# Optimization experiments

Measured on AMD Instinct MI355X. Metric: run time of the kernel, lower is better.

The kernel has to match this reference:

```python
import jax, jax.numpy as jnp
import numpy as np

D_MODEL = 1024
BATCH = 4
SEQ = 4096

def setup_inputs() -> dict:
    key = jax.random.key(0)
    k1, k2, k3, k4 = jax.random.split(key, 4)
    scale = 1.0 / np.sqrt(D_MODEL)
    return {
        "inp_emb": jax.random.normal(k1, (BATCH, SEQ, D_MODEL), dtype=jnp.float32),
        "Wq": jax.random.normal(k2, (D_MODEL, D_MODEL), dtype=jnp.float32) * scale,
        "Wk": jax.random.normal(k3, (D_MODEL, D_MODEL), dtype=jnp.float32) * scale,
        "Wv": jax.random.normal(k4, (D_MODEL, D_MODEL), dtype=jnp.float32) * scale,
    }

def reference(inp_emb, Wq, Wk, Wv):
    d_model = Wq.shape[0]
    # torch Linear (no bias): y = x @ W.T
    Q = jnp.einsum('bsd,ed->bse', inp_emb, Wq)
    K = jnp.einsum('bsd,ed->bse', inp_emb, Wk)
    V = jnp.einsum('bsd,ed->bse', inp_emb, Wv)
    scores = jnp.einsum('bqd,bkd->bqk', Q, K) / jnp.sqrt(jnp.float32(d_model))
    probs = jax.nn.softmax(scores, axis=2)
    return jnp.einsum('bqk,bkd->bqd', probs, V)
```

## Files before the change

kernel.cpp:

```cpp
#include <hip/hip_runtime.h>


typedef __bf16 bf16_t;
typedef __bf16 bf16x8 __attribute__((ext_vector_type(8)));
typedef float f32x4 __attribute__((ext_vector_type(4)));

typedef __attribute__((address_space(3))) void lds_void_t;
typedef __attribute__((address_space(1))) void gbl_void_t;

#define SEQ 4096
#define DM  1024

__global__ __launch_bounds__(256) void cast_f32_to_bf16(
    const float* __restrict__ in, bf16_t* __restrict__ out, int n8)
{
    int idx = blockIdx.x * 256 + threadIdx.x;
    if (idx >= n8) return;
    long i = (long)idx * 8;
    f32x4 a = *(const f32x4*)(in + i);
    f32x4 b = *(const f32x4*)(in + i + 4);
    bf16x8 o;
    o[0] = (bf16_t)a[0]; o[1] = (bf16_t)a[1]; o[2] = (bf16_t)a[2]; o[3] = (bf16_t)a[3];
    o[4] = (bf16_t)b[0]; o[5] = (bf16_t)b[1]; o[6] = (bf16_t)b[2]; o[7] = (bf16_t)b[3];
    *(bf16x8*)(out + i) = o;
}

__global__ __launch_bounds__(256) void cast3_w(
    const float* __restrict__ w0, const float* __restrict__ w1,
    const float* __restrict__ w2, bf16_t* __restrict__ out)
{
    const float* in = (blockIdx.z == 0) ? w0 : (blockIdx.z == 1) ? w1 : w2;
    long i = ((long)blockIdx.x * 256 + threadIdx.x) * 8;
    f32x4 a = *(const f32x4*)(in + i);
    f32x4 b = *(const f32x4*)(in + i + 4);
    bf16x8 o;
    o[0] = (bf16_t)a[0]; o[1] = (bf16_t)a[1]; o[2] = (bf16_t)a[2]; o[3] = (bf16_t)a[3];
    o[4] = (bf16_t)b[0]; o[5] = (bf16_t)b[1]; o[6] = (bf16_t)b[2]; o[7] = (bf16_t)b[3];
    *(bf16x8*)(out + (long)blockIdx.z * 1048576 + i) = o;
}

__global__ __launch_bounds__(256) void zero_f32(float* __restrict__ p, int n)
{
    int idx = blockIdx.x * 256 + threadIdx.x;
    if (idx < n) p[idx] = 0.f;
}

template <typename TOUT, int MODE>
__global__ __launch_bounds__(256, 4) void gemm_bt(
    const bf16_t* __restrict__ A, int lda, long sAz,
    const bf16_t* __restrict__ B, int ldb, long sBz,
    TOUT* __restrict__ C, int ldc, long sCz,
    int K, float scale, float* __restrict__ l, long sLz)
{
    __shared__ bf16_t As[128 * 32];
    __shared__ bf16_t Bs[128 * 32];

    A += (long)blockIdx.z * sAz;
    B += (long)blockIdx.z * sBz;
    C += (long)blockIdx.z * sCz;

    const int tid  = threadIdx.x;
    const int wave = tid >> 6;
    const int lane = tid & 63;
    const int m0 = blockIdx.x * 128;
    const int n0 = blockIdx.y * 128;
    const int wm = (wave >> 1) * 64;
    const int wn = (wave & 1) * 64;
    const int mrow = lane & 15;
    const int koff = (lane >> 4) * 8;

    f32x4 acc[4][4];
#pragma unroll
    for (int i = 0; i < 4; ++i)
#pragma unroll
        for (int j = 0; j < 4; ++j)
            acc[i][j] = (f32x4){0.f, 0.f, 0.f, 0.f};

    const int c0 = wave * 2;

    for (int k0 = 0; k0 < K; k0 += 32) {
#pragma unroll
        for (int t = 0; t < 2; ++t) {
            const int chunk = c0 + t;
            const int flat  = chunk * 64 + lane;
            const int row   = flat >> 2;
            const int kp    = (flat & 3) * 8;
            const bf16_t* ga = A + (long)(m0 + row) * lda + (k0 + kp);
            const bf16_t* gb = B + (long)(n0 + row) * ldb + (k0 + kp);
            __builtin_amdgcn_global_load_lds((const gbl_void_t*)ga,
                                             (lds_void_t*)(As + chunk * 512), 16, 0, 0);
            __builtin_amdgcn_global_load_lds((const gbl_void_t*)gb,
                                             (lds_void_t*)(Bs + chunk * 512), 16, 0, 0);
        }
        __syncthreads();

        bf16x8 af[4], bfr[4];
#pragma unroll
        for (int i = 0; i < 4; ++i)
            af[i] = *(const bf16x8*)(As + (wm + i * 16 + mrow) * 32 + koff);
#pragma unroll
        for (int j = 0; j < 4; ++j)
            bfr[j] = *(const bf16x8*)(Bs + (wn + j * 16 + mrow) * 32 + koff);
#pragma unroll
        for (int i = 0; i < 4; ++i)
#pragma unroll
            for (int j = 0; j < 4; ++j)
                acc[i][j] = __builtin_amdgcn_mfma_f32_16x16x32_bf16(af[i], bfr[j], acc[i][j], 0, 0, 0);
        __syncthreads();
    }

    const int col = lane & 15;
    const int r0  = (lane >> 4) * 4;

    if (MODE == 1) {
#pragma unroll
        for (int i = 0; i < 4; ++i)
#pragma unroll
            for (int r = 0; r < 4; ++r) {
                float s = 0.f;
#pragma unroll
                for (int j = 0; j < 4; ++j) {
                    float e = __expf(acc[i][j][r] * scale);
                    acc[i][j][r] = e;
                    s += e;
                }
                s += __shfl_xor(s, 1);
                s += __shfl_xor(s, 2);
                s += __shfl_xor(s, 4);
                s += __shfl_xor(s, 8);
                if (col == 0)
                    atomicAdd(&l[(long)blockIdx.z * sLz + m0 + wm + i * 16 + r0 + r], s);
            }
#pragma unroll
        for (int i = 0; i < 4; ++i)
#pragma unroll
            for (int j = 0; j < 4; ++j)
#pragma unroll
                for (int r = 0; r < 4; ++r)
                    C[(long)(m0 + wm + i * 16 + r0 + r) * ldc + (n0 + wn + j * 16 + col)] =
                        (TOUT)acc[i][j][r];
    } else if (MODE == 2) {
        float inv[4][4];
#pragma unroll
        for (int i = 0; i < 4; ++i)
#pragma unroll
            for (int r = 0; r < 4; ++r)
                inv[i][r] = scale / l[(long)blockIdx.z * sLz + m0 + wm + i * 16 + r0 + r];
#pragma unroll
        for (int i = 0; i < 4; ++i)
#pragma unroll
            for (int j = 0; j < 4; ++j)
#pragma unroll
                for (int r = 0; r < 4; ++r)
                    C[(long)(m0 + wm + i * 16 + r0 + r) * ldc + (n0 + wn + j * 16 + col)] =
                        (TOUT)(acc[i][j][r] * inv[i][r]);
    } else {
#pragma unroll
        for (int i = 0; i < 4; ++i)
#pragma unroll
            for (int j = 0; j < 4; ++j)
#pragma unroll
                for (int r = 0; r < 4; ++r)
                    C[(long)(m0 + wm + i * 16 + r0 + r) * ldc + (n0 + wn + j * 16 + col)] =
                        (TOUT)(acc[i][j][r] * scale);
    }
}

template <typename TOUT, int MODE, int LDA, int LDB, int LDC>
__global__ __launch_bounds__(512, 4) void gemm_bt256(
    const bf16_t* __restrict__ A, long sAz,
    const bf16_t* __restrict__ B, long sBz,
    TOUT* __restrict__ C, long sCz,
    int K, float scale, float* __restrict__ l, long sLz)
{
    __shared__ __align__(1024) char smem[73728];

    A += (long)blockIdx.z * sAz;
    B += (long)blockIdx.z * sBz;
    C += (long)blockIdx.z * sCz;

    const int tid  = threadIdx.x;
    const int wave = tid >> 6;
    const int lane = tid & 63;
    const int m0 = blockIdx.x * 256;
    const int n0 = blockIdx.y * 128;
    const int wm = (wave >> 2) * 128;
    const int wn = (wave & 3) * 32;

    const int srow = wave * 16 + (lane >> 2);
    const int ksrc = (((lane & 3) ^ ((lane >> 3) & 3)) << 3);
    const bf16_t* pa0 = A + (long)(m0 + srow) * LDA + ksrc;
    const bf16_t* pa1 = pa0 + (long)128 * LDA;
    const bf16_t* pb0 = B + (long)(n0 + srow) * LDB + ksrc;
    const int ldsw = wave * 1024;

    const int kterm = (((lane >> 4) ^ ((lane >> 1) & 3)) << 4);
    const int aoff = (wm + (lane & 15)) * 64 + kterm;
    const int boff = (wn + (lane & 15)) * 64 + kterm;

    f32x4 acc[8][2];
#pragma unroll
    for (int i = 0; i < 8; ++i)
#pragma unroll
        for (int j = 0; j < 2; ++j)
            acc[i][j] = (f32x4){0.f, 0.f, 0.f, 0.f};

    const int NT = K >> 5;

#define STAGE_A2(buf)                                                          \
    do {                                                                       \
        __builtin_amdgcn_global_load_lds((const gbl_void_t*)pa0,               \
            (lds_void_t*)(smem + (buf)*16384 + ldsw), 16, 0, 0);               \
        __builtin_amdgcn_global_load_lds((const gbl_void_t*)pa1,               \
            (lds_void_t*)(smem + (buf)*16384 + 8192 + ldsw), 16, 0, 0);        \
    } while (0)
#define STAGE_B1(buf)                                                          \
    __builtin_amdgcn_global_load_lds((const gbl_void_t*)pb0,                   \
        (lds_void_t*)(smem + 49152 + (buf)*8192 + ldsw), 16, 0, 0)

    STAGE_A2(0); STAGE_B1(0); pa0 += 32; pa1 += 32; pb0 += 32;
    if (NT > 1) {
        STAGE_A2(1); STAGE_B1(1); pa0 += 32; pa1 += 32; pb0 += 32;
        asm volatile("s_waitcnt vmcnt(3)" ::: "memory");
    } else {
        asm volatile("s_waitcnt vmcnt(0)" ::: "memory");
    }
    __builtin_amdgcn_sched_barrier(0);
    __builtin_amdgcn_s_barrier();

    int cur = 0, sb = 2;
    for (int t = 0; t < NT; ++t) {
        const char* Ab = smem + cur * 16384;
        const char* Bb = smem + 49152 + cur * 8192;
        const bool more = (t + 2 < NT);

        bf16x8 bfr[2], af[4];
#pragma unroll
        for (int j = 0; j < 2; ++j) bfr[j] = *(const bf16x8*)(Bb + boff + j * 1024);
#pragma unroll
        for (int i = 0; i < 4; ++i) af[i] = *(const bf16x8*)(Ab + aoff + i * 1024);
        if (more) STAGE_A2(sb);
        asm volatile("s_waitcnt lgkmcnt(0)" ::: "memory");
        __builtin_amdgcn_sched_barrier(0);
        __builtin_amdgcn_s_setprio(1);
#pragma unroll
        for (int i = 0; i < 4; ++i)
#pragma unroll
            for (int j = 0; j < 2; ++j)
                acc[i][j] = __builtin_amdgcn_mfma_f32_16x16x32_bf16(af[i], bfr[j], acc[i][j], 0, 0, 0);
        __builtin_amdgcn_s_setprio(0);

#pragma unroll
        for (int i = 0; i < 4; ++i) af[i] = *(const bf16x8*)(Ab + aoff + 4096 + i * 1024);
        if (more) STAGE_B1(sb);
        asm volatile("s_waitcnt lgkmcnt(0)" ::: "memory");
        __builtin_amdgcn_sched_barrier(0);
        __builtin_amdgcn_s_setprio(1);
#pragma unroll
        for (int i = 0; i < 4; ++i)
#pragma unroll
            for (int j = 0; j < 2; ++j)
                acc[4 + i][j] = __builtin_amdgcn_mfma_f32_16x16x32_bf16(af[i], bfr[j], acc[4 + i][j], 0, 0, 0);
        __builtin_amdgcn_s_setprio(0);

        if (more) {
            asm volatile("s_waitcnt vmcnt(3)" ::: "memory");
            pa0 += 32; pa1 += 32; pb0 += 32;
        } else if (t + 1 < NT) {
            asm volatile("s_waitcnt vmcnt(0)" ::: "memory");
        }
        __builtin_amdgcn_sched_barrier(0);
        __builtin_amdgcn_s_barrier();
        cur = (cur == 2) ? 0 : cur + 1;
        sb  = (sb == 2) ? 0 : sb + 1;
    }
#undef STAGE_A2
#undef STAGE_B1

    const int col = lane & 15;
    const int r0  = (lane >> 4) * 4;

    if (MODE == 1) {
#pragma unroll
        for (int i = 0; i < 8; ++i)
#pragma unroll
            for (int r = 0; r < 4; ++r) {
                float s = 0.f;
#pragma unroll
                for (int j = 0; j < 2; ++j) {
                    float e = __expf(acc[i][j][r] * scale);
                    acc[i][j][r] = e;
                    s += e;
                }
                s += __shfl_xor(s, 1);
                s += __shfl_xor(s, 2);
                s += __shfl_xor(s, 4);
                s += __shfl_xor(s, 8);
                if (col == 0)
                    atomicAdd(&l[(long)blockIdx.z * sLz + m0 + wm + i * 16 + r0 + r], s);
            }
#pragma unroll
        for (int i = 0; i < 8; ++i)
#pragma unroll
            for (int j = 0; j < 2; ++j)
#pragma unroll
                for (int r = 0; r < 4; ++r)
                    C[(long)(m0 + wm + i * 16 + r0 + r) * LDC + (n0 + wn + j * 16 + col)] =
                        (TOUT)acc[i][j][r];
    } else if (MODE == 2) {
        float inv[8][4];
#pragma unroll
        for (int i = 0; i < 8; ++i)
#pragma unroll
            for (int r = 0; r < 4; ++r)
                inv[i][r] = scale / l[(long)blockIdx.z * sLz + m0 + wm + i * 16 + r0 + r];
#pragma unroll
        for (int i = 0; i < 8; ++i)
#pragma unroll
            for (int j = 0; j < 2; ++j)
#pragma unroll
                for (int r = 0; r < 4; ++r)
                    C[(long)(m0 + wm + i * 16 + r0 + r) * LDC + (n0 + wn + j * 16 + col)] =
                        (TOUT)(acc[i][j][r] * inv[i][r]);
    } else {
#pragma unroll
        for (int i = 0; i < 8; ++i)
#pragma unroll
            for (int j = 0; j < 2; ++j)
#pragma unroll
                for (int r = 0; r < 4; ++r)
                    C[(long)(m0 + wm + i * 16 + r0 + r) * LDC + (n0 + wn + j * 16 + col)] =
                        (TOUT)(acc[i][j][r] * scale);
    }
}

__device__ __forceinline__ float waveMax(float v)
{
#pragma unroll
    for (int o = 32; o > 0; o >>= 1) v = fmaxf(v, __shfl_xor(v, o));
    return v;
}
__device__ __forceinline__ float waveSum(float v)
{
#pragma unroll
    for (int o = 32; o > 0; o >>= 1) v += __shfl_xor(v, o);
    return v;
}

__global__ __launch_bounds__(256) void softmax_rows(bf16_t* __restrict__ S)
{
    const long row = blockIdx.x;
    bf16_t* p = S + row * SEQ;
    const int tid = threadIdx.x;

    float v[16];
    bf16x8 a0 = *(const bf16x8*)(p + tid * 16);
    bf16x8 a1 = *(const bf16x8*)(p + tid * 16 + 8);
#pragma unroll
    for (int i = 0; i < 8; ++i) { v[i] = (float)a0[i]; v[8 + i] = (float)a1[i]; }

    float m = -1e30f;
#pragma unroll
    for (int i = 0; i < 16; ++i) m = fmaxf(m, v[i]);

    __shared__ float redm[4];
    __shared__ float reds[4];
    m = waveMax(m);
    if ((tid & 63) == 0) redm[tid >> 6] = m;
    __syncthreads();
    m = fmaxf(fmaxf(redm[0], redm[1]), fmaxf(redm[2], redm[3]));

    float s = 0.f;
#pragma unroll
    for (int i = 0; i < 16; ++i) { v[i] = __expf(v[i] - m); s += v[i]; }
    s = waveSum(s);
    if ((tid & 63) == 0) reds[tid >> 6] = s;
    __syncthreads();
    s = reds[0] + reds[1] + reds[2] + reds[3];
    const float inv = 1.0f / s;

    bf16x8 o0, o1;
#pragma unroll
    for (int i = 0; i < 8; ++i) {
        o0[i] = (bf16_t)(v[i] * inv);
        o1[i] = (bf16_t)(v[8 + i] * inv);
    }
    *(bf16x8*)(p + tid * 16)     = o0;
    *(bf16x8*)(p + tid * 16 + 8) = o1;
}

__global__ __launch_bounds__(256) void transpose_bf16(
    const bf16_t* __restrict__ in, int ldin, long sInZ,
    bf16_t* __restrict__ out, int ldout, long sOutZ)
{
    in  += (long)blockIdx.z * sInZ;
    out += (long)blockIdx.z * sOutZ;
    __shared__ bf16_t t[32][33];
    const int tx = threadIdx.x;
    const int ty = threadIdx.y;
    const int x  = blockIdx.x * 32 + tx;
    const int y0 = blockIdx.y * 32;
#pragma unroll
    for (int i = 0; i < 4; ++i)
        t[ty + i * 8][tx] = in[(long)(y0 + ty + i * 8) * ldin + x];
    __syncthreads();
    const int xo = blockIdx.x * 32;
#pragma unroll
    for (int i = 0; i < 4; ++i)
        out[(long)(xo + ty + i * 8) * ldout + y0 + tx] = t[tx][ty + i * 8];
}

extern "C" void kernel_launch(void* const* d_in, const int* in_sizes, int n_in,
                              void* d_out, int out_size, void* d_ws, size_t ws_size,
                              hipStream_t stream)
{
    const float* X  = (const float*)d_in[0];
    const float* Wq = (const float*)d_in[1];
    const float* Wk = (const float*)d_in[2];
    const float* Wv = (const float*)d_in[3];
    float* out = (float*)d_out;
    char* ws = (char*)d_ws;

    if (ws_size >= (256ull << 20)) {
        bf16_t* Xbf  = (bf16_t*)ws;
        bf16_t* Vbf  = (bf16_t*)(ws + (32l << 20));
        bf16_t* Tbuf = (bf16_t*)(ws + (32l << 20));
        bf16_t* VT   = (bf16_t*)(ws + (64l << 20));
        bf16_t* Sbuf = (bf16_t*)(ws + (96l << 20));
        bf16_t* Wall = (bf16_t*)(ws + (224l << 20));
        bf16_t* WqT  = (bf16_t*)(ws + (230l << 20));
        bf16_t* WkT  = (bf16_t*)(ws + (232l << 20));
        bf16_t* Mt   = (bf16_t*)(ws + (234l << 20));
        float*  lbuf = (float*)(ws + (236l << 20));

        cast_f32_to_bf16<<<(16777216 / 8) / 256, 256, 0, stream>>>(X, Xbf, 16777216 / 8);
        cast3_w<<<dim3(512, 1, 3), 256, 0, stream>>>(Wq, Wk, Wv, Wall);

        transpose_bf16<<<dim3(32, 32, 2), dim3(32, 8), 0, stream>>>(
            Wall, DM, 1048576, WqT, DM, 1048576);

        gemm_bt<bf16_t, 0><<<dim3(8, 8, 1), 256, 0, stream>>>(
            WkT, DM, 0l, WqT, DM, 0l, Mt, DM, 0l, DM, 1.0f, nullptr, 0l);

        gemm_bt256<bf16_t, 0, DM, DM, DM><<<dim3(64, 8, 1), 512, 0, stream>>>(
            Xbf, 0l, Wall + 2097152, 0l, Vbf, 0l, DM, 1.0f, nullptr, 0l);

        transpose_bf16<<<dim3(DM / 32, SEQ / 32, 4), dim3(32, 8), 0, stream>>>(
            Vbf, DM, (long)SEQ * DM, VT, SEQ, (long)DM * SEQ);

        gemm_bt256<bf16_t, 0, DM, DM, DM><<<dim3(64, 8, 1), 512, 0, stream>>>(
            Xbf, 0l, Mt, 0l, Tbuf, 0l, DM, 1.0f, nullptr, 0l);

        zero_f32<<<64, 256, 0, stream>>>(lbuf, 4 * SEQ);

        gemm_bt256<bf16_t, 1, DM, DM, SEQ><<<dim3(16, 32, 4), 512, 0, stream>>>(
            Tbuf, (long)SEQ * DM,
            Xbf, (long)SEQ * DM,
            Sbuf, (long)SEQ * SEQ, DM, 0.03125f, lbuf, SEQ);

        gemm_bt256<float, 2, SEQ, SEQ, DM><<<dim3(16, 8, 4), 512, 0, stream>>>(
            Sbuf, (long)SEQ * SEQ,
            VT, (long)DM * SEQ,
            out, (long)SEQ * DM, SEQ, 1.0f, lbuf, SEQ);
    } else {
        bf16_t* Sbuf = (bf16_t*)ws;
        bf16_t* Xbf  = (bf16_t*)ws;
        bf16_t* Wall = (bf16_t*)(ws + (33l << 20));
        bf16_t* QKV  = (bf16_t*)(ws + (40l << 20));
        bf16_t* VT   = (bf16_t*)(ws + (137l << 20));

        cast_f32_to_bf16<<<(16777216 / 8) / 256, 256, 0, stream>>>(X, Xbf, 16777216 / 8);
        cast3_w<<<dim3(512, 1, 3), 256, 0, stream>>>(Wq, Wk, Wv, Wall);

        gemm_bt<bf16_t, 0><<<dim3(128, 24, 1), 256, 0, stream>>>(
            Xbf, DM, 0l, Wall, DM, 0l, QKV, 3072, 0l, DM, 1.0f, nullptr, 0l);

        for (int b = 0; b < 4; ++b) {
            const bf16_t* Qb = QKV + (long)b * SEQ * 3072;
            gemm_bt<bf16_t, 0><<<dim3(32, 32, 1), 256, 0, stream>>>(
                Qb, 3072, 0l, Qb + 1024, 3072, 0l, Sbuf, SEQ, 0l, DM, 0.03125f, nullptr, 0l);
            softmax_rows<<<SEQ, 256, 0, stream>>>(Sbuf);
            transpose_bf16<<<dim3(DM / 32, SEQ / 32, 1), dim3(32, 8), 0, stream>>>(
                Qb + 2048, 3072, 0l, VT, SEQ, 0l);
            gemm_bt<float, 0><<<dim3(32, 8, 1), 256, 0, stream>>>(
                Sbuf, SEQ, 0l, VT, SEQ, 0l, out + (long)b * SEQ * DM, DM, 0l, SEQ, 1.0f, nullptr, 0l);
        }
    }
}
```

Measured before the change: 545.7 us.

## Add 256x256 projection GEMM computing V transposed directly, swizzle block order

Adds a new 256x256-tile double-buffered projection GEMM kernel with direct global-to-LDS loads. It computes V^T directly as Wv·X^T per batch, which removes the separate V projection write plus transpose pass. It also uses this kernel for the X·M projection and adds a grouped workgroup-order swizzle to the existing 256x128 GEMM to improve L2 reuse. The costs are larger LDS use (128KB, lower occupancy) and strided output writes for VT.

```diff
diff --git a/kernel.cpp b/kernel.cpp
--- a/kernel.cpp
+++ b/kernel.cpp
@@ -166,6 +166,160 @@
     }
 }
 
+__global__ __launch_bounds__(512, 2) void gemm_proj(
+    const bf16_t* __restrict__ A, int lda, long sAz,
+    const bf16_t* __restrict__ B, int ldb, long sBz,
+    bf16_t* __restrict__ C, int ldc, long sCz,
+    int K, float scale)
+{
+    __shared__ __align__(1024) char smem[131072];
+
+    A += (long)blockIdx.z * sAz;
+    B += (long)blockIdx.z * sBz;
+    C += (long)blockIdx.z * sCz;
+
+    const int wg  = blockIdx.y * gridDim.x + blockIdx.x;
+    const int qq  = (gridDim.x * gridDim.y) >> 3;
+    const int sw  = (wg & 7) * qq + (wg >> 3);
+    const int m0 = (sw % gridDim.x) * 256;
+    const int n0 = (sw / gridDim.x) * 256;
+
+    const int tid  = threadIdx.x;
+    const int wave = tid >> 6;
+    const int lane = tid & 63;
+    const int wm = (wave >> 2) * 128;
+    const int wn = (wave & 3) * 64;
+
+    const int ksw = ((lane & 7) ^ (lane >> 3)) * 8;
+    const bf16_t* gAr = A + (long)(m0 + wave * 8 + (lane >> 3)) * lda + ksw;
+    const bf16_t* gBr = B + (long)(n0 + wave * 8 + (lane >> 3)) * ldb + ksw;
+    const int ldsw = wave * 1024;
+
+    const int kterm = ((lane >> 4) * 16) ^ ((lane & 7) << 4);
+    const int aoff = (wm + (lane & 15)) * 128 + kterm;
+    const int boff = (wn + (lane & 15)) * 128 + kterm;
+
+    f32x4 acc[8][4];
+#pragma unroll
+    for (int i = 0; i < 8; ++i)
+#pragma unroll
+        for (int j = 0; j < 4; ++j)
+            acc[i][j] = (f32x4){0.f, 0.f, 0.f, 0.f};
+
+    const int NT = K >> 6;
+
+#define STAGE_A(buf, k0e, s)                                                   \
+    __builtin_amdgcn_global_load_lds(                                          \
+        (const gbl_void_t*)(gAr + (long)(s)*64 * lda + (k0e)),                 \
+        (lds_void_t*)(smem + (buf)*32768 + (s)*8192 + ldsw), 16, 0, 0)
+#define STAGE_B(buf, k0e, s)                                                   \
+    __builtin_amdgcn_global_load_lds(                                          \
+        (const gbl_void_t*)(gBr + (long)(s)*64 * ldb + (k0e)),                 \
+        (lds_void_t*)(smem + 65536 + (buf)*32768 + (s)*8192 + ldsw), 16, 0, 0)
+
+    STAGE_B(0, 0, 0); STAGE_B(0, 0, 1); STAGE_B(0, 0, 2); STAGE_B(0, 0, 3);
+    STAGE_A(0, 0, 0); STAGE_A(0, 0, 2); STAGE_A(0, 0, 1); STAGE_A(0, 0, 3);
+    asm volatile("s_waitcnt vmcnt(2)" ::: "memory");
+    __builtin_amdgcn_sched_barrier(0);
+    __builtin_amdgcn_s_barrier();
+
+    for (int t = 0; t < NT; ++t) {
+        const int cb = t & 1;
+        const int nb = cb ^ 1;
+        const char* Ac = smem + cb * 32768;
+        const char* Bc = smem + 65536 + cb * 32768;
+        const bool more = (t + 1 < NT);
+        const int kn = (t + 1) << 6;
+
+        bf16x8 b0[4], b1[4], af[4];
+
+#pragma unroll
+        for (int j = 0; j < 4; ++j) b0[j] = *(const bf16x8*)(Bc + boff + j * 2048);
+#pragma unroll
+        for (int i = 0; i < 4; ++i) af[i] = *(const bf16x8*)(Ac + aoff + i * 2048);
+        if (more) { STAGE_B(nb, kn, 0); STAGE_B(nb, kn, 1); }
+        __builtin_amdgcn_s_barrier();
+        asm volatile("s_waitcnt lgkmcnt(0)" ::: "memory");
+        __builtin_amdgcn_sched_barrier(0);
+        __builtin_amdgcn_s_setprio(1);
+#pragma unroll
+        for (int i = 0; i < 4; ++i)
+#pragma unroll
+            for (int j = 0; j < 4; ++j)
+                acc[i][j] = __builtin_amdgcn_mfma_f32_16x16x32_bf16(af[i], b0[j], acc[i][j], 0, 0, 0);
+        __builtin_amdgcn_s_setprio(0);
+        __builtin_amdgcn_s_barrier();
+
+#pragma unroll
+        for (int j = 0; j < 4; ++j) b1[j] = *(const bf16x8*)(Bc + (boff ^ 64) + j * 2048);
+#pragma unroll
+        for (int i = 0; i < 4; ++i) af[i] = *(const bf16x8*)(Ac + (aoff ^ 64) + i * 2048);
+        if (more) { STAGE_B(nb, kn, 2); STAGE_B(nb, kn, 3); }
+        __builtin_amdgcn_s_barrier();
+        asm volatile("s_waitcnt lgkmcnt(0)" ::: "memory");
+        __builtin_amdgcn_sched_barrier(0);
+        __builtin_amdgcn_s_setprio(1);
+#pragma unroll
+        for (int i = 0; i < 4; ++i)
+#pragma unroll
+            for (int j = 0; j < 4; ++j)
+                acc[i][j] = __builtin_amdgcn_mfma_f32_16x16x32_bf16(af[i], b1[j], acc[i][j], 0, 0, 0);
+        __builtin_amdgcn_s_setprio(0);
+        if (more)
+            asm volatile("s_waitcnt vmcnt(4)" ::: "memory");
+        else
+            asm volatile("s_waitcnt vmcnt(0)" ::: "memory");
+        __builtin_amdgcn_sched_barrier(0);
+        __builtin_amdgcn_s_barrier();
+
+#pragma unroll
+        for (int i = 0; i < 4; ++i) af[i] = *(const bf16x8*)(Ac + aoff + 8192 + i * 2048);
+        if (more) { STAGE_A(nb, kn, 0); STAGE_A(nb, kn, 2); }
+        __builtin_amdgcn_s_barrier();
+        asm volatile("s_waitcnt lgkmcnt(0)" ::: "memory");
+        __builtin_amdgcn_sched_barrier(0);
+        __builtin_amdgcn_s_setprio(1);
+#pragma unroll
+        for (int i = 0; i < 4; ++i)
+#pragma unroll
+            for (int j = 0; j < 4; ++j)
+                acc[4 + i][j] = __builtin_amdgcn_mfma_f32_16x16x32_bf16(af[i], b0[j], acc[4 + i][j], 0, 0, 0);
+        __builtin_amdgcn_s_setprio(0);
+        __builtin_amdgcn_s_barrier();
+
+#pragma unroll
+        for (int i = 0; i < 4; ++i) af[i] = *(const bf16x8*)(Ac + (aoff ^ 64) + 8192 + i * 2048);
+        if (more) { STAGE_A(nb, kn, 1); STAGE_A(nb, kn, 3); }
+        __builtin_amdgcn_s_barrier();
+        asm volatile("s_waitcnt lgkmcnt(0)" ::: "memory");
+        __builtin_amdgcn_sched_barrier(0);
+        __builtin_amdgcn_s_setprio(1);
+#pragma unroll
+        for (int i = 0; i < 4; ++i)
+#pragma unroll
+            for (int j = 0; j < 4; ++j)
+                acc[4 + i][j] = __builtin_amdgcn_mfma_f32_16x16x32_bf16(af[i], b1[j], acc[4 + i][j], 0, 0, 0);
+        __builtin_amdgcn_s_setprio(0);
+        if (more)
+            asm volatile("s_waitcnt vmcnt(2)" ::: "memory");
+        __builtin_amdgcn_sched_barrier(0);
+        __builtin_amdgcn_s_barrier();
+    }
+#undef STAGE_A
+#undef STAGE_B
+
+    const int col = lane & 15;
+    const int r0  = (lane >> 4) * 4;
+#pragma unroll
+    for (int i = 0; i < 8; ++i)
+#pragma unroll
+        for (int j = 0; j < 4; ++j)
+#pragma unroll
+            for (int r = 0; r < 4; ++r)
+                C[(long)(m0 + wm + i * 16 + r0 + r) * ldc + (n0 + wn + j * 16 + col)] =
+                    (bf16_t)(acc[i][j][r] * scale);
+}
+
 template <typename TOUT, int MODE, int LDA, int LDB, int LDC>
 __global__ __launch_bounds__(512, 4) void gemm_bt256(
     const bf16_t* __restrict__ A, long sAz,
@@ -179,11 +333,15 @@
     B += (long)blockIdx.z * sBz;
     C += (long)blockIdx.z * sCz;
 
+    const int wg  = blockIdx.y * gridDim.x + blockIdx.x;
+    const int qq  = (gridDim.x * gridDim.y) >> 3;
+    const int sw  = (wg & 7) * qq + (wg >> 3);
+    const int m0 = (sw % gridDim.x) * 256;
+    const int n0 = (sw / gridDim.x) * 128;
+
     const int tid  = threadIdx.x;
     const int wave = tid >> 6;
     const int lane = tid & 63;
-    const int m0 = blockIdx.x * 256;
-    const int n0 = blockIdx.y * 128;
     const int wm = (wave >> 2) * 128;
     const int wn = (wave & 3) * 32;
 
@@ -423,7 +581,6 @@
 
     if (ws_size >= (256ull << 20)) {
         bf16_t* Xbf  = (bf16_t*)ws;
-        bf16_t* Vbf  = (bf16_t*)(ws + (32l << 20));
         bf16_t* Tbuf = (bf16_t*)(ws + (32l << 20));
         bf16_t* VT   = (bf16_t*)(ws + (64l << 20));
         bf16_t* Sbuf = (bf16_t*)(ws + (96l << 20));
@@ -442,14 +599,13 @@
         gemm_bt<bf16_t, 0><<<dim3(8, 8, 1), 256, 0, stream>>>(
             WkT, DM, 0l, WqT, DM, 0l, Mt, DM, 0l, DM, 1.0f, nullptr, 0l);
 
-        gemm_bt256<bf16_t, 0, DM, DM, DM><<<dim3(64, 8, 1), 512, 0, stream>>>(
-            Xbf, 0l, Wall + 2097152, 0l, Vbf, 0l, DM, 1.0f, nullptr, 0l);
-
-        transpose_bf16<<<dim3(DM / 32, SEQ / 32, 4), dim3(32, 8), 0, stream>>>(
-            Vbf, DM, (long)SEQ * DM, VT, SEQ, (long)DM * SEQ);
-
-        gemm_bt256<bf16_t, 0, DM, DM, DM><<<dim3(64, 8, 1), 512, 0, stream>>>(
-            Xbf, 0l, Mt, 0l, Tbuf, 0l, DM, 1.0f, nullptr, 0l);
+        gemm_proj<<<dim3(4, 16, 4), 512, 0, stream>>>(
+            Wall + 2097152, DM, 0l,
+            Xbf, DM, (long)SEQ * DM,
+            VT, SEQ, (long)DM * SEQ, DM, 1.0f);
+
+        gemm_proj<<<dim3(64, 4, 1), 512, 0, stream>>>(
+            Xbf, DM, 0l, Mt, DM, 0l, Tbuf, DM, 0l, DM, 1.0f);
 
         zero_f32<<<64, 256, 0, stream>>>(lbuf, 4 * SEQ);
 
```

Result: slower. 578.1 us (+5.9%).
